# Performance work log

Measured on AMD Instinct MI355X. Metric: run time of the kernel, lower is better.

The kernel has to match this reference:

```python
import jax, jax.numpy as jnp
import numpy as np

K = 64
PI = np.float32(np.pi)


def setup_inputs() -> dict:
    key = jax.random.key(0)
    k1, k2 = jax.random.split(key)
    B, N = 4096, 21
    rotation = jax.random.normal(k1, (B, N, 3, 3), dtype=jnp.float32)
    conditions = jax.random.normal(k2, (B, N, 4 * K), dtype=jnp.float32)
    permute = np.arange(3).astype(np.int64)  # static permutation indices
    return {"rotation": rotation, "conditions": conditions, "permute": permute}


def _mobius_forward(rotation, conditions, p0, p1, p2):
    B, N = rotation.shape[0], rotation.shape[1]
    I3 = jnp.eye(3, dtype=rotation.dtype)

    x = rotation[..., p0]  # [B,N,3]
    y = rotation[..., p1]  # [B,N,3]

    # compute_mcl_parameters_nd
    weights = conditions[..., :K]                      # [B,N,K]
    w = conditions[..., K:].reshape(B, N, K, 3)        # [B,N,K,3]
    proj = I3 - jnp.einsum('bni,bnj->bnij', y, y)      # [B,N,3,3]
    w = jnp.einsum('bnij,bnkj->bnki', proj, w)
    r = -x
    r = r / jnp.linalg.norm(r, axis=-1, keepdims=True)
    v = jnp.cross(y, r)
    v = v / jnp.linalg.norm(v, axis=-1, keepdims=True)
    weights = jax.nn.softplus(weights)
    weights = weights / jnp.sum(weights, axis=-1, keepdims=True)
    w_norm = jnp.linalg.norm(w, axis=-1, keepdims=True)
    w = 0.7 / (1.0 + w_norm) * w

    # _forward_nd
    z = x
    zw = z[:, :, None, :] - w                          # [B,N,K,3]
    zw_norm = jnp.linalg.norm(zw, axis=-1)             # [B,N,K]
    w_norm2 = jnp.sum(w * w, axis=-1)                  # [B,N,K]
    h_z = ((1.0 - w_norm2) / zw_norm ** 2)[..., None] * zw - w  # [B,N,K,3]

    radians = jnp.arctan2(jnp.einsum('bnki,bni->bnk', h_z, v),
                          jnp.einsum('bnki,bni->bnk', h_z, r))
    ang = jnp.where(radians >= 0, radians, radians + 2.0 * PI)
    ang = jnp.sum(weights * ang, axis=2, keepdims=True)          # [B,N,1]
    tx = r * jnp.cos(ang) + v * jnp.sin(ang)                     # [B,N,3]

    zw_unit = zw / zw_norm[..., None]
    theta = jnp.arctan2(jnp.einsum('bni,bni->bn', x, v),
                        jnp.einsum('bni,bni->bn', x, r))[..., None]  # [B,N,1]
    dz_dtheta = -jnp.sin(theta) * r + jnp.cos(theta) * v             # [B,N,3]
    dh_dz = (1.0 - w_norm2)[..., None, None] * (
        I3 - 2.0 * jnp.einsum('bnki,bnkj->bnkij', zw_unit, zw_unit)
    ) / (zw_norm ** 2)[..., None, None]                              # [B,N,K,3,3]
    dh_dtheta = jnp.einsum('bnkpq,bnq->bnkp', dh_dz, dz_dtheta)      # [B,N,K,3]
    dtx = jnp.sum(jnp.linalg.norm(dh_dtheta, axis=-1) * weights, axis=2)  # [B,N]
    ldj = jnp.log(dtx)

    if (p1 - p0 == 1) or (p1 - p0 == -2):
        tz = jnp.cross(tx, y)
    else:
        tz = jnp.cross(y, tx)
    tz = tz / jnp.linalg.norm(tz, axis=-1, keepdims=True)

    cols = [None, None, None]
    cols[p0] = tx
    cols[p1] = y
    cols[p2] = tz
    trotation = jnp.stack(cols, axis=-1)  # [B,N,3,3]
    return trotation, jnp.sum(ldj, axis=-1)


def reference(rotation, conditions, permute):
    p0, p1, p2 = int(permute[0]), int(permute[1]), int(permute[2])
    return _mobius_forward(rotation, conditions, p0, p1, p2)
```

## Files before the change

### kernel.cpp

```cpp
#include <hip/hip_runtime.h>
#include <math.h>

#define PI_F    3.14159265358979323846f
#define TWO_PI  6.28318530717958647692f
#define HALF_PI 1.57079632679489661923f

__device__ __forceinline__ float frcp(float x)  { return __builtin_amdgcn_rcpf(x); }
__device__ __forceinline__ float frsq(float x)  { return __builtin_amdgcn_rsqf(x); }
__device__ __forceinline__ float fsqrt(float x) { return __builtin_amdgcn_sqrtf(x); }

__device__ __forceinline__ float fast_atan2_2pi(float y, float x) {
    float ax = fabsf(x), ay = fabsf(y);
    float mx = fmaxf(ax, ay), mn = fminf(ax, ay);
    float a  = (mx > 0.0f) ? mn * frcp(mx) : 0.0f;
    float s  = a * a;
    float r  = fmaf(s, fmaf(s, fmaf(s, fmaf(s, 0.0208351f, -0.085133f),
                                    0.180141f), -0.3302995f), 0.9998660f) * a;
    if (ay > ax) r = HALF_PI - r;
    if (x < 0.0f) r = PI_F - r;
    return (y < 0.0f) ? (TWO_PI - r) : r;
}

__global__ __launch_bounds__(448, 4)
void mobius_fwd(const float* __restrict__ rot,
                const float* __restrict__ cond,
                const void* __restrict__ perm,
                float* __restrict__ out,
                int B, int N)
{
    const int wave = threadIdx.x >> 6;
    const int lane = threadIdx.x & 63;
    const int sub  = lane >> 3;
    const int j    = lane & 7;
    const int nwav = blockDim.x >> 6;

    const int b0   = blockIdx.x * 8;
    const int nb   = min(8, B - b0);
    const int nit  = N * nb;
    const int noct = (nit + 7) >> 3;

    const int* pi = (const int*)perm;
    int p0 = pi[0], p1 = pi[1], p2 = pi[2];
    bool pok = ((unsigned)p0 < 3u) && ((unsigned)p1 < 3u) && ((unsigned)p2 < 3u)
               && (p0 != p1) && (p0 != p2) && (p1 != p2);
    if (!pok) {
        const long long* pl = (const long long*)perm;
        p0 = (int)pl[0]; p1 = (int)pl[1]; p2 = (int)pl[2];
    }
    const int dd = p1 - p0;
    const bool swapc = (dd == 1 || dd == -2);

    __shared__ float s_ldj[192];

    const size_t base_item = (size_t)b0 * N;

    for (int q = wave; q < noct; q += nwav) {
        const int  i0    = 8 * q + sub;
        const bool valid = (i0 < nit);
        const size_t item = base_item + (valid ? i0 : 0);

        const float* C = cond + item * 256;
        float4 pwa = *(const float4*)(C + 8 * j);
        float4 pwb = *(const float4*)(C + 8 * j + 4);
        const float* W = C + 64 + 24 * j;
        float4 f0 = ((const float4*)W)[0];
        float4 f1 = ((const float4*)W)[1];
        float4 f2 = ((const float4*)W)[2];
        float4 f3 = ((const float4*)W)[3];
        float4 f4 = ((const float4*)W)[4];
        float4 f5 = ((const float4*)W)[5];

        const float* R = rot + item * 9;
        float x0 = R[p0], x1 = R[3 + p0], x2 = R[6 + p0];
        float y0 = R[p1], y1 = R[3 + p1], y2 = R[6 + p1];

        float xn2    = x0 * x0 + x1 * x1 + x2 * x2;
        float inv_xn = frsq(xn2);
        float xn     = xn2 * inv_xn;
        float xy     = x0 * y0 + x1 * y1 + x2 * y2;
        float yn2    = y0 * y0 + y1 * y1 + y2 * y2;
        float negA   = yn2 - 2.0f;

        float cv0 = x1 * y2 - x2 * y1;
        float cv1 = x2 * y0 - x0 * y2;
        float cv2 = x0 * y1 - x1 * y0;
        float inv_cn = frsq(cv0 * cv0 + cv1 * cv1 + cv2 * cv2);
        float v0 = cv0 * inv_cn, v1 = cv1 * inv_cn, v2 = cv2 * inv_cn;

        float PW[8] = {pwa.x, pwa.y, pwa.z, pwa.w, pwb.x, pwb.y, pwb.z, pwb.w};
        float W0[8] = {f0.x, f0.w, f1.z, f2.y, f3.x, f3.w, f4.z, f5.y};
        float W1[8] = {f0.y, f1.x, f1.w, f2.z, f3.y, f4.x, f4.w, f5.z};
        float W2[8] = {f0.z, f1.y, f2.x, f2.w, f3.z, f4.y, f5.x, f5.w};

        float pp = 0.0f, pa = 0.0f, pd = 0.0f;
        #pragma unroll
        for (int cc = 0; cc < 8; ++cc) {
            float w0 = W0[cc], w1 = W1[cc], w2 = W2[cc];
            float yw  = y0 * w0 + y1 * w1 + y2 * w2;
            float wp2 = w0 * w0 + w1 * w1 + w2 * w2;
            float xwp = x0 * w0 + x1 * w1 + x2 * w2;
            float vwp = v0 * w0 + v1 * w1 + v2 * w2;
            float qn2 = fmaxf(fmaf(yw * yw, negA, wp2), 0.0f);
            float sc  = 0.7f * frcp(1.0f + fsqrt(qn2));
            float wn2 = (sc * sc) * qn2;
            float xw  = sc * fmaf(-xy, yw, xwp);
            float zwn2 = fmaf(-2.0f, xw, xn2 + wn2);
            float c   = (1.0f - wn2) * frcp(zwn2);
            float cp1 = c + 1.0f;
            float hv  = -(cp1 * (sc * vwp));
            float hr  = fmaf(cp1, xw * inv_xn, -(c * xn));
            float ang = fast_atan2_2pi(hv, hr);
            float p   = __logf(1.0f + __expf(PW[cc]));
            pp += p; pa = fmaf(p, ang, pa); pd = fmaf(p, c, pd);
        }

        #pragma unroll
        for (int off = 4; off >= 1; off >>= 1) {
            pp += __shfl_xor(pp, off, 64);
            pa += __shfl_xor(pa, off, 64);
            pd += __shfl_xor(pd, off, 64);
        }

        if (j == 0 && valid) {
            float ip   = frcp(pp);
            float angT = pa * ip;
            float ldj  = __logf(pd * ip);

            float sa, ca;
            __sincosf(angT, &sa, &ca);
            float r0 = -x0 * inv_xn, r1 = -x1 * inv_xn, r2 = -x2 * inv_xn;
            float t0 = fmaf(r0, ca, v0 * sa);
            float t1 = fmaf(r1, ca, v1 * sa);
            float t2 = fmaf(r2, ca, v2 * sa);

            float u0, u1, u2;
            if (swapc) {
                u0 = t1 * y2 - t2 * y1;
                u1 = t2 * y0 - t0 * y2;
                u2 = t0 * y1 - t1 * y0;
            } else {
                u0 = y1 * t2 - y2 * t1;
                u1 = y2 * t0 - y0 * t2;
                u2 = y0 * t1 - y1 * t0;
            }
            float iun = frsq(u0 * u0 + u1 * u1 + u2 * u2);
            u0 *= iun; u1 *= iun; u2 *= iun;

            float* T = out + item * 9;
            T[p0] = t0; T[3 + p0] = t1; T[6 + p0] = t2;
            T[p1] = y0; T[3 + p1] = y1; T[6 + p1] = y2;
            T[p2] = u0; T[3 + p2] = u1; T[6 + p2] = u2;

            s_ldj[i0] = ldj;
        }
    }

    __syncthreads();
    if (threadIdx.x < nb) {
        float acc = 0.0f;
        for (int n = 0; n < N; ++n) acc += s_ldj[threadIdx.x * N + n];
        out[(size_t)B * N * 9 + b0 + threadIdx.x] = acc;
    }
}

extern "C" void kernel_launch(void* const* d_in, const int* in_sizes, int n_in,
                              void* d_out, int out_size, void* d_ws, size_t ws_size,
                              hipStream_t stream) {
    const float* rot  = (const float*)d_in[0];
    const float* cond = (const float*)d_in[1];
    const void*  perm = d_in[2];
    float* out = (float*)d_out;

    int items = in_sizes[0] / 9;
    int B = out_size - items * 9;
    int N = items / B;

    int grid = (B + 7) / 8;
    mobius_fwd<<<dim3(grid), dim3(448), 0, stream>>>(rot, cond, perm, out, B, N);
}
```

Baseline: 25.66 us.

## Split into flat per-item kernel plus separate ldj reduction kernel

When workspace is large enough, the work is split into two kernels. The first maps one 8-lane group to each item across a flat grid of 256-thread blocks and writes per-item ldj to workspace. The second sums ldj over N per batch element. This removes the per-batch block granularity and the partially idle 448-thread blocks, at the cost of a second launch and an extra global round trip for ldj. The original fused kernel stays as a fallback.

Result: slower. 35.55 us (+38.5%).

```diff
diff --git a/kernel.cpp b/kernel.cpp
--- a/kernel.cpp
+++ b/kernel.cpp
@@ -21,12 +21,162 @@
     return (y < 0.0f) ? (TWO_PI - r) : r;
 }
 
+__device__ __forceinline__ void item_body(
+    const float* __restrict__ rot, const float* __restrict__ cond,
+    float* __restrict__ out, size_t item, int j,
+    int p0, int p1, int p2, bool swapc, float* ldj_out)
+{
+    const float* C = cond + item * 256;
+    float4 pwa = *(const float4*)(C + 8 * j);
+    float4 pwb = *(const float4*)(C + 8 * j + 4);
+    const float* W = C + 64 + 24 * j;
+    float4 f0 = ((const float4*)W)[0];
+    float4 f1 = ((const float4*)W)[1];
+    float4 f2 = ((const float4*)W)[2];
+    float4 f3 = ((const float4*)W)[3];
+    float4 f4 = ((const float4*)W)[4];
+    float4 f5 = ((const float4*)W)[5];
+
+    const float* R = rot + item * 9;
+    float x0 = R[p0], x1 = R[3 + p0], x2 = R[6 + p0];
+    float y0 = R[p1], y1 = R[3 + p1], y2 = R[6 + p1];
+
+    float xn2    = x0 * x0 + x1 * x1 + x2 * x2;
+    float inv_xn = frsq(xn2);
+    float xn     = xn2 * inv_xn;
+    float xy     = x0 * y0 + x1 * y1 + x2 * y2;
+    float yn2    = y0 * y0 + y1 * y1 + y2 * y2;
+    float negA   = yn2 - 2.0f;
+
+    float cv0 = x1 * y2 - x2 * y1;
+    float cv1 = x2 * y0 - x0 * y2;
+    float cv2 = x0 * y1 - x1 * y0;
+    float inv_cn = frsq(cv0 * cv0 + cv1 * cv1 + cv2 * cv2);
+    float v0 = cv0 * inv_cn, v1 = cv1 * inv_cn, v2 = cv2 * inv_cn;
+
+    float PW[8] = {pwa.x, pwa.y, pwa.z, pwa.w, pwb.x, pwb.y, pwb.z, pwb.w};
+    float W0[8] = {f0.x, f0.w, f1.z, f2.y, f3.x, f3.w, f4.z, f5.y};
+    float W1[8] = {f0.y, f1.x, f1.w, f2.z, f3.y, f4.x, f4.w, f5.z};
+    float W2[8] = {f0.z, f1.y, f2.x, f2.w, f3.z, f4.y, f5.x, f5.w};
+
+    float pp = 0.0f, pa = 0.0f, pd = 0.0f;
+    #pragma unroll
+    for (int cc = 0; cc < 8; ++cc) {
+        float w0 = W0[cc], w1 = W1[cc], w2 = W2[cc];
+        float yw  = y0 * w0 + y1 * w1 + y2 * w2;
+        float wp2 = w0 * w0 + w1 * w1 + w2 * w2;
+        float xwp = x0 * w0 + x1 * w1 + x2 * w2;
+        float vwp = v0 * w0 + v1 * w1 + v2 * w2;
+        float qn2 = fmaxf(fmaf(yw * yw, negA, wp2), 0.0f);
+        float sc  = 0.7f * frcp(1.0f + fsqrt(qn2));
+        float wn2 = (sc * sc) * qn2;
+        float xw  = sc * fmaf(-xy, yw, xwp);
+        float zwn2 = fmaf(-2.0f, xw, xn2 + wn2);
+        float c   = (1.0f - wn2) * frcp(zwn2);
+        float cp1 = c + 1.0f;
+        float hv  = -(cp1 * (sc * vwp));
+        float hr  = fmaf(cp1, xw * inv_xn, -(c * xn));
+        float ang = fast_atan2_2pi(hv, hr);
+        float p   = __logf(1.0f + __expf(PW[cc]));
+        pp += p; pa = fmaf(p, ang, pa); pd = fmaf(p, c, pd);
+    }
+
+    #pragma unroll
+    for (int off = 4; off >= 1; off >>= 1) {
+        pp += __shfl_xor(pp, off, 64);
+        pa += __shfl_xor(pa, off, 64);
+        pd += __shfl_xor(pd, off, 64);
+    }
+
+    float ip   = frcp(pp);
+    float angT = pa * ip;
+    *ldj_out   = __logf(pd * ip);
+
+    if (j == 0) {
+        float sa, ca;
+        __sincosf(angT, &sa, &ca);
+        float r0 = -x0 * inv_xn, r1 = -x1 * inv_xn, r2 = -x2 * inv_xn;
+        float t0 = fmaf(r0, ca, v0 * sa);
+        float t1 = fmaf(r1, ca, v1 * sa);
+        float t2 = fmaf(r2, ca, v2 * sa);
+
+        float u0, u1, u2;
+        if (swapc) {
+            u0 = t1 * y2 - t2 * y1;
+            u1 = t2 * y0 - t0 * y2;
+            u2 = t0 * y1 - t1 * y0;
+        } else {
+            u0 = y1 * t2 - y2 * t1;
+            u1 = y2 * t0 - y0 * t2;
+            u2 = y0 * t1 - y1 * t0;
+        }
+        float iun = frsq(u0 * u0 + u1 * u1 + u2 * u2);
+        u0 *= iun; u1 *= iun; u2 *= iun;
+
+        float* T = out + item * 9;
+        T[p0] = t0; T[3 + p0] = t1; T[6 + p0] = t2;
+        T[p1] = y0; T[3 + p1] = y1; T[6 + p1] = y2;
+        T[p2] = u0; T[3 + p2] = u1; T[6 + p2] = u2;
+    }
+}
+
+__device__ __forceinline__ void read_perm(const void* perm, int& p0, int& p1, int& p2) {
+    const int* pi = (const int*)perm;
+    p0 = pi[0]; p1 = pi[1]; p2 = pi[2];
+    bool pok = ((unsigned)p0 < 3u) && ((unsigned)p1 < 3u) && ((unsigned)p2 < 3u)
+               && (p0 != p1) && (p0 != p2) && (p1 != p2);
+    if (!pok) {
+        const long long* pl = (const long long*)perm;
+        p0 = (int)pl[0]; p1 = (int)pl[1]; p2 = (int)pl[2];
+    }
+}
+
+__global__ __launch_bounds__(256, 8)
+void mobius_main(const float* __restrict__ rot,
+                 const float* __restrict__ cond,
+                 const void* __restrict__ perm,
+                 float* __restrict__ out,
+                 float* __restrict__ ws,
+                 int total_items)
+{
+    const int wave = threadIdx.x >> 6;
+    const int lane = threadIdx.x & 63;
+    const int sub  = lane >> 3;
+    const int j    = lane & 7;
+
+    int p0, p1, p2;
+    read_perm(perm, p0, p1, p2);
+    const int dd = p1 - p0;
+    const bool swapc = (dd == 1 || dd == -2);
+
+    const long long oct = (long long)blockIdx.x * 4 + wave;
+    const long long it  = oct * 8 + sub;
+    if (it >= total_items) return;
+    const size_t item = (size_t)it;
+
+    float ldj;
+    item_body(rot, cond, out, item, j, p0, p1, p2, swapc, &ldj);
+    if (j == 0) ws[item] = ldj;
+}
+
+__global__ __launch_bounds__(256)
+void ldj_reduce(const float* __restrict__ ws, float* __restrict__ out,
+                int B, int N, long long out_off)
+{
+    int b = blockIdx.x * 256 + threadIdx.x;
+    if (b >= B) return;
+    const float* p = ws + (size_t)b * N;
+    float acc = 0.0f;
+    for (int n = 0; n < N; ++n) acc += p[n];
+    out[out_off + b] = acc;
+}
+
 __global__ __launch_bounds__(448, 4)
-void mobius_fwd(const float* __restrict__ rot,
-                const float* __restrict__ cond,
-                const void* __restrict__ perm,
-                float* __restrict__ out,
-                int B, int N)
+void mobius_fused(const float* __restrict__ rot,
+                  const float* __restrict__ cond,
+                  const void* __restrict__ perm,
+                  float* __restrict__ out,
+                  int B, int N)
 {
     const int wave = threadIdx.x >> 6;
     const int lane = threadIdx.x & 63;
@@ -39,120 +189,21 @@
     const int nit  = N * nb;
     const int noct = (nit + 7) >> 3;
 
-    const int* pi = (const int*)perm;
-    int p0 = pi[0], p1 = pi[1], p2 = pi[2];
-    bool pok = ((unsigned)p0 < 3u) && ((unsigned)p1 < 3u) && ((unsigned)p2 < 3u)
-               && (p0 != p1) && (p0 != p2) && (p1 != p2);
-    if (!pok) {
-        const long long* pl = (const long long*)perm;
-        p0 = (int)pl[0]; p1 = (int)pl[1]; p2 = (int)pl[2];
-    }
+    int p0, p1, p2;
+    read_perm(perm, p0, p1, p2);
     const int dd = p1 - p0;
     const bool swapc = (dd == 1 || dd == -2);
 
     __shared__ float s_ldj[192];
-
     const size_t base_item = (size_t)b0 * N;
 
     for (int q = wave; q < noct; q += nwav) {
         const int  i0    = 8 * q + sub;
         const bool valid = (i0 < nit);
         const size_t item = base_item + (valid ? i0 : 0);
-
-        const float* C = cond + item * 256;
-        float4 pwa = *(const float4*)(C + 8 * j);
-        float4 pwb = *(const float4*)(C + 8 * j + 4);
-        const float* W = C + 64 + 24 * j;
-        float4 f0 = ((const float4*)W)[0];
-        float4 f1 = ((const float4*)W)[1];
-        float4 f2 = ((const float4*)W)[2];
-        float4 f3 = ((const float4*)W)[3];
-        float4 f4 = ((const float4*)W)[4];
-        float4 f5 = ((const float4*)W)[5];
-
-        const float* R = rot + item * 9;
-        float x0 = R[p0], x1 = R[3 + p0], x2 = R[6 + p0];
-        float y0 = R[p1], y1 = R[3 + p1], y2 = R[6 + p1];
-
-        float xn2    = x0 * x0 + x1 * x1 + x2 * x2;
-        float inv_xn = frsq(xn2);
-        float xn     = xn2 * inv_xn;
-        float xy     = x0 * y0 + x1 * y1 + x2 * y2;
-        float yn2    = y0 * y0 + y1 * y1 + y2 * y2;
-        float negA   = yn2 - 2.0f;
-
-        float cv0 = x1 * y2 - x2 * y1;
-        float cv1 = x2 * y0 - x0 * y2;
-        float cv2 = x0 * y1 - x1 * y0;
-        float inv_cn = frsq(cv0 * cv0 + cv1 * cv1 + cv2 * cv2);
-        float v0 = cv0 * inv_cn, v1 = cv1 * inv_cn, v2 = cv2 * inv_cn;
-
-        float PW[8] = {pwa.x, pwa.y, pwa.z, pwa.w, pwb.x, pwb.y, pwb.z, pwb.w};
-        float W0[8] = {f0.x, f0.w, f1.z, f2.y, f3.x, f3.w, f4.z, f5.y};
-        float W1[8] = {f0.y, f1.x, f1.w, f2.z, f3.y, f4.x, f4.w, f5.z};
-        float W2[8] = {f0.z, f1.y, f2.x, f2.w, f3.z, f4.y, f5.x, f5.w};
-
-        float pp = 0.0f, pa = 0.0f, pd = 0.0f;
-        #pragma unroll
-        for (int cc = 0; cc < 8; ++cc) {
-            float w0 = W0[cc], w1 = W1[cc], w2 = W2[cc];
-            float yw  = y0 * w0 + y1 * w1 + y2 * w2;
-            float wp2 = w0 * w0 + w1 * w1 + w2 * w2;
-            float xwp = x0 * w0 + x1 * w1 + x2 * w2;
-            float vwp = v0 * w0 + v1 * w1 + v2 * w2;
-            float qn2 = fmaxf(fmaf(yw * yw, negA, wp2), 0.0f);
-            float sc  = 0.7f * frcp(1.0f + fsqrt(qn2));
-            float wn2 = (sc * sc) * qn2;
-            float xw  = sc * fmaf(-xy, yw, xwp);
-            float zwn2 = fmaf(-2.0f, xw, xn2 + wn2);
-            float c   = (1.0f - wn2) * frcp(zwn2);
-            float cp1 = c + 1.0f;
-            float hv  = -(cp1 * (sc * vwp));
-            float hr  = fmaf(cp1, xw * inv_xn, -(c * xn));
-            float ang = fast_atan2_2pi(hv, hr);
-            float p   = __logf(1.0f + __expf(PW[cc]));
-            pp += p; pa = fmaf(p, ang, pa); pd = fmaf(p, c, pd);
-        }
-
-        #pragma unroll
-        for (int off = 4; off >= 1; off >>= 1) {
-            pp += __shfl_xor(pp, off, 64);
-            pa += __shfl_xor(pa, off, 64);
-            pd += __shfl_xor(pd, off, 64);
-        }
-
-        if (j == 0 && valid) {
-            float ip   = frcp(pp);
-            float angT = pa * ip;
-            float ldj  = __logf(pd * ip);
-
-            float sa, ca;
-            __sincosf(angT, &sa, &ca);
-            float r0 = -x0 * inv_xn, r1 = -x1 * inv_xn, r2 = -x2 * inv_xn;
-            float t0 = fmaf(r0, ca, v0 * sa);
-            float t1 = fmaf(r1, ca, v1 * sa);
-            float t2 = fmaf(r2, ca, v2 * sa);
-
-            float u0, u1, u2;
-            if (swapc) {
-                u0 = t1 * y2 - t2 * y1;
-                u1 = t2 * y0 - t0 * y2;
-                u2 = t0 * y1 - t1 * y0;
-            } else {
-                u0 = y1 * t2 - y2 * t1;
-                u1 = y2 * t0 - y0 * t2;
-                u2 = y0 * t1 - y1 * t0;
-            }
-            float iun = frsq(u0 * u0 + u1 * u1 + u2 * u2);
-            u0 *= iun; u1 *= iun; u2 *= iun;
-
-            float* T = out + item * 9;
-            T[p0] = t0; T[3 + p0] = t1; T[6 + p0] = t2;
-            T[p1] = y0; T[3 + p1] = y1; T[6 + p1] = y2;
-            T[p2] = u0; T[3 + p2] = u1; T[6 + p2] = u2;
-
-            s_ldj[i0] = ldj;
-        }
+        float ldj;
+        item_body(rot, cond, out, item, j, p0, p1, p2, swapc, &ldj);
+        if (j == 0 && valid) s_ldj[i0] = ldj;
     }
 
     __syncthreads();
@@ -175,6 +226,16 @@
     int B = out_size - items * 9;
     int N = items / B;
 
-    int grid = (B + 7) / 8;
-    mobius_fwd<<<dim3(grid), dim3(448), 0, stream>>>(rot, cond, perm, out, B, N);
-}
+    if (ws_size >= (size_t)items * sizeof(float)) {
+        long long octs = ((long long)items + 7) / 8;
+        int grid1 = (int)((octs + 3) / 4);
+        mobius_main<<<dim3(grid1), dim3(256), 0, stream>>>(
+            rot, cond, perm, out, (float*)d_ws, items);
+        int grid2 = (B + 255) / 256;
+        ldj_reduce<<<dim3(grid2), dim3(256), 0, stream>>>(
+            (const float*)d_ws, out, B, N, (long long)items * 9);
+    } else {
+        int grid = (B + 7) / 8;
+        mobius_fused<<<dim3(grid), dim3(448), 0, stream>>>(rot, cond, perm, out, B, N);
+    }
+}
```
